# Kernel tuning notes

Measured on AMD Instinct MI355X. Metric: run time of the kernel, lower is better.

Reference implementation:

```python
import jax, jax.numpy as jnp
import numpy as np

DIM_HEAD = 32  # from init_kwargs; scale = dim_head**-0.5 per the Triton kernel


def setup_inputs() -> dict:
    key = jax.random.key(0)
    k1, k2 = jax.random.split(key)
    B, N, dim = 16, 8192, 128
    D = 4 * DIM_HEAD  # heads * dim_head
    x = jax.random.normal(k1, (B, N, dim), dtype=jnp.float32)
    # ParameterList of 16 stages, each Parameter is randn(2, dim, D) * 0.02
    qk_weights = jax.random.normal(k2, (16, 2, dim, D), dtype=jnp.float32) * 0.02
    return {"x": x, "qk_weights": qk_weights}


def reference(x, qk_weights):
    """FFT-inspired butterfly attention.

    At stage s (stride = 2**s), positions are grouped into blocks of 2*stride;
    the first `stride` elements of each block are 'a', the next `stride` are
    their butterfly partners 'b' (b = a + stride). Q/K are projected from the
    ORIGINAL x with per-stage weights; v is the running value buffer (init x).
    For each pair, a 2-way softmax over [qa.ka, qa.kb] mixes (va, vb).
    """
    B, N, dim = x.shape
    logN = int(round(np.log2(N)))
    D = qk_weights.shape[-1]
    scale = DIM_HEAD ** -0.5

    v = x
    for s in range(logN):
        stride = 1 << s
        Wq = qk_weights[s, 0]  # (dim, D)
        Wk = qk_weights[s, 1]
        q = jnp.einsum('bnd,de->bne', x, Wq) * scale  # (B,N,D)
        k = jnp.einsum('bnd,de->bne', x, Wk)
        G = N // (2 * stride)
        qr = q.reshape(B, G, 2, stride, D)
        kr = k.reshape(B, G, 2, stride, D)
        vr = v.reshape(B, G, 2, stride, dim)
        qa = qr[:, :, 0]
        ka, kb = kr[:, :, 0], kr[:, :, 1]
        va, vb = vr[:, :, 0], vr[:, :, 1]
        s_aa = jnp.sum(qa * ka, axis=-1)  # (B,G,stride)
        s_ab = jnp.sum(qa * kb, axis=-1)
        attn = jax.nn.softmax(jnp.stack([s_aa, s_ab], axis=-1), axis=-1)
        w0 = attn[..., 0:1]
        w1 = attn[..., 1:2]
        out_a = w0 * va + w1 * vb
        out_b = w1 * va + w0 * vb
        v = jnp.stack([out_a, out_b], axis=2).reshape(B, N, dim)
    return v
```

## Files before the change

### kernel.cpp

```cpp
#include <hip/hip_runtime.h>
#include <hip/hip_bf16.h>


typedef __bf16 bf16x8 __attribute__((ext_vector_type(8)));
typedef float  f32x4  __attribute__((ext_vector_type(4)));

#define XSTR 136
#define XB_BYTES  (128 * XSTR * 2)
#define PREP_LDS  (2 * XB_BYTES)
#define LDS_W     XB_BYTES

#define VSTR 132
#define LDS_MIX (128 * VSTR * 4)

#define WS_DWT_OFF (512 * 1024)
#define DWT8_BYTES (13 * 1024 * 8 * 64 * 4)
#define DWT2_BYTES (13 * 1024 * 128 * 4)
#define WS_NEED8   (WS_DWT_OFF + DWT8_BYTES)
#define WS_NEED2   (WS_DWT_OFF + DWT2_BYTES)

__device__ __forceinline__ float ubits(unsigned int u) {
    union { unsigned int u; float f; } v; v.u = u; return v.f;
}
__device__ __forceinline__ unsigned short f2bf(float f) {
    union { float f; unsigned int u; } v; v.f = f;
    unsigned int u = v.u;
    return (unsigned short)((u + 0x7fffu + ((u >> 16) & 1u)) >> 16);
}

#define DPP_MOV_F(x, ctrl) \
    __int_as_float(__builtin_amdgcn_update_dpp(0, __float_as_int(x), (ctrl), 0xF, 0xF, true))

__device__ __forceinline__ float xlane_u(float x, int u, int lane) {
    if (u == 0) return DPP_MOV_F(x, 0xB1);
    if (u == 1) return DPP_MOV_F(x, 0x4E);
    if (u == 2) return __int_as_float(__builtin_amdgcn_ds_swizzle(__float_as_int(x), 0x101F));
    if (u == 3) return __int_as_float(__builtin_amdgcn_ds_swizzle(__float_as_int(x), 0x201F));
    if (u == 4) return __int_as_float(__builtin_amdgcn_ds_swizzle(__float_as_int(x), 0x401F));
    return __int_as_float(__builtin_amdgcn_ds_bpermute((lane ^ 32) << 2, __float_as_int(x)));
}

__global__ __launch_bounds__(512)
void prep_kernel(const float* __restrict__ qkw, unsigned short* __restrict__ PT) {
    extern __shared__ char smem[];
    unsigned short* wkb = (unsigned short*)smem;
    unsigned short* wqb = (unsigned short*)(smem + XB_BYTES);
    const int s = blockIdx.x;
    const float* Wq = qkw + (size_t)s * 32768;
    const float* Wk = Wq + 16384;
    const int tid = threadIdx.x;
    const int rl = tid >> 5, c4 = tid & 31;
#pragma unroll
    for (int j = 0; j < 8; ++j) {
        int r = j * 16 + rl;
        float4 vq = ((const float4*)Wq)[r * 32 + c4];
        float4 vk = ((const float4*)Wk)[r * 32 + c4];
        ushort4 uq; uq.x = f2bf(vq.x); uq.y = f2bf(vq.y); uq.z = f2bf(vq.z); uq.w = f2bf(vq.w);
        ushort4 uk; uk.x = f2bf(vk.x); uk.y = f2bf(vk.y); uk.z = f2bf(vk.z); uk.w = f2bf(vk.w);
        *(ushort4*)(wqb + r * XSTR + c4 * 4) = uq;
        *(ushort4*)(wkb + r * XSTR + c4 * 4) = uk;
    }
    __syncthreads();
    const int lane = tid & 63, w = tid >> 6;
    const int lane15 = lane & 15, quad = lane >> 4;
    f32x4 acc[8] = {};
#pragma unroll
    for (int kk = 0; kk < 4; ++kk) {
        bf16x8 a = *(const bf16x8*)(wkb + (w * 16 + lane15) * XSTR + kk * 32 + quad * 8);
#pragma unroll
        for (int ct = 0; ct < 8; ++ct) {
            bf16x8 b = *(const bf16x8*)(wqb + (ct * 16 + lane15) * XSTR + kk * 32 + quad * 8);
            acc[ct] = __builtin_amdgcn_mfma_f32_16x16x32_bf16(a, b, acc[ct], 0, 0, 0);
        }
    }
    unsigned short* dst = PT + s * 16384;
#pragma unroll
    for (int ct = 0; ct < 8; ++ct) {
        const int kkf = ct >> 1;
        const int qf  = (ct & 1) * 2 + (lane15 >> 3);
        const int e   = lane15 & 7;
#pragma unroll
        for (int r = 0; r < 4; ++r) {
            int fi = (w * 4 + kkf) * 64 + qf * 16 + quad * 4 + r;
            dst[fi * 8 + e] = f2bf(acc[ct][r] * 0.17677669529663687f);
        }
    }
}

__device__ __forceinline__ void stage_xb(unsigned short* xb, const float* xsrc,
                                         int tid, int base, int h_off, int rstride) {
    const int rl = tid >> 5, c4 = tid & 31;
#pragma unroll
    for (int j = 0; j < 8; ++j) {
        int i  = j * 16 + rl;
        int gp = base + (i >> 6) * h_off + (i & 63) * rstride;
        float4 val = ((const float4*)xsrc)[gp * 32 + c4];
        ushort4 us; us.x = f2bf(val.x); us.y = f2bf(val.y);
        us.z = f2bf(val.z); us.w = f2bf(val.w);
        *(ushort4*)(xb + i * XSTR + c4 * 4) = us;
    }
}

template<int NS>
__global__ __launch_bounds__(512, 4)
void weights8_kernel(const float* __restrict__ xsrc,
                     const unsigned short* __restrict__ PT,
                     float* __restrict__ dwt,
                     int s0, int base_mul, int h_off, int rstride)
{
    extern __shared__ char smem[];
    unsigned short* xb = (unsigned short*)smem;

    const int tid  = threadIdx.x;
    const int b    = blockIdx.x >> 6;
    const int sub  = blockIdx.x & 63;
    const int base = b * 8192 + sub * base_mul;

    stage_xb(xb, xsrc, tid, base, h_off, rstride);

    const int lane = tid & 63, w = tid >> 6;
    const int lane15 = lane & 15, quad = lane >> 4;

    __syncthreads();

#pragma unroll
    for (int u = 0; u < NS; ++u) {
        const int t   = 1 << u;
        const int tm1 = t - 1;

        const uint4* Pf = (const uint4*)PT + (size_t)(s0 + u) * 2048;
        uint4 af[4];
#pragma unroll
        for (int kk = 0; kk < 4; ++kk)
            af[kk] = Pf[(w * 4 + kk) * 64 + lane];

        f32x4 acc[4] = {};
#pragma unroll
        for (int pg = 0; pg < 4; ++pg) {
            const int p  = pg * 16 + lane15;
            const int ar = ((p & ~tm1) << 1) | (p & tm1);
            const unsigned short* brow = xb + ar * XSTR + quad * 8;
#pragma unroll
            for (int kk = 0; kk < 4; ++kk) {
                bf16x8 bfrag = *(const bf16x8*)(brow + kk * 32);
                union { uint4 u; bf16x8 b; } av; av.u = af[kk];
                acc[pg] = __builtin_amdgcn_mfma_f32_16x16x32_bf16(av.b, bfrag, acc[pg], 0, 0, 0);
            }
        }

        float sm[4];
#pragma unroll
        for (int pg = 0; pg < 4; ++pg) {
            const int p  = pg * 16 + lane15;
            const int ar = ((p & ~tm1) << 1) | (p & tm1);
            const unsigned short* da = xb + ar * XSTR + w * 16 + quad * 4;
            const unsigned short* db = da + t * XSTR;
            uint2 ua = *(const uint2*)da;
            uint2 ub = *(const uint2*)db;
            float a0 = ubits(ua.x << 16), a1 = ubits(ua.x & 0xffff0000u);
            float a2 = ubits(ua.y << 16), a3 = ubits(ua.y & 0xffff0000u);
            float b0 = ubits(ub.x << 16), b1 = ubits(ub.x & 0xffff0000u);
            float b2 = ubits(ub.y << 16), b3 = ubits(ub.y & 0xffff0000u);
            float s = acc[pg][0] * (a0 - b0) + acc[pg][1] * (a1 - b1)
                    + acc[pg][2] * (a2 - b2) + acc[pg][3] * (a3 - b3);
            s += xlane_u(s, 4, lane);
            s += xlane_u(s, 5, lane);
            sm[pg] = s;
        }
        float v = (lane & 32) ? ((lane & 16) ? sm[3] : sm[2])
                              : ((lane & 16) ? sm[1] : sm[0]);
        dwt[(((size_t)(s0 + u) * 1024 + blockIdx.x) * 8 + w) * 64 + lane] = v;
    }
}

template<int NS>
__global__ __launch_bounds__(512, 4)
void weights2_kernel(const float* __restrict__ xsrc,
                     const unsigned short* __restrict__ PT,
                     float* __restrict__ dwt,
                     int s0, int base_mul, int h_off, int rstride)
{
    extern __shared__ char smem[];
    unsigned short* xb = (unsigned short*)smem;

    const int tid  = threadIdx.x;
    const int b    = blockIdx.x >> 6;
    const int sub  = blockIdx.x & 63;
    const int base = b * 8192 + sub * base_mul;

    stage_xb(xb, xsrc, tid, base, h_off, rstride);

    const int lane = tid & 63, w = tid >> 6;
    const int lane15 = lane & 15, quad = lane >> 4;
    const int nt = w & 3;
    const int mh = w >> 2;
    const int p  = nt * 16 + lane15;

    __syncthreads();

#pragma unroll
    for (int u = 0; u < NS; ++u) {
        const int t   = 1 << u;
        const int tm1 = t - 1;
        const int ar  = ((p & ~tm1) << 1) | (p & tm1);

        float sm = 0.f;
        {
            const uint4* Pf = (const uint4*)PT + (size_t)(s0 + u) * 2048;
            const unsigned short* brow = xb + ar * XSTR + quad * 8;
            f32x4 acc[4] = {};
#pragma unroll
            for (int kk = 0; kk < 4; ++kk) {
                bf16x8 bfrag = *(const bf16x8*)(brow + kk * 32);
#pragma unroll
                for (int mt = 0; mt < 4; ++mt) {
                    union { uint4 u; bf16x8 b; } av;
                    av.u = Pf[((mh * 4 + mt) * 4 + kk) * 64 + lane];
                    acc[mt] = __builtin_amdgcn_mfma_f32_16x16x32_bf16(av.b, bfrag, acc[mt], 0, 0, 0);
                }
            }
            const unsigned short* da = xb + ar * XSTR + mh * 64 + quad * 4;
            const unsigned short* db = da + t * XSTR;
#pragma unroll
            for (int mt = 0; mt < 4; ++mt) {
                uint2 ua = *(const uint2*)(da + mt * 16);
                uint2 ub = *(const uint2*)(db + mt * 16);
                float a0 = ubits(ua.x << 16), a1 = ubits(ua.x & 0xffff0000u);
                float a2 = ubits(ua.y << 16), a3 = ubits(ua.y & 0xffff0000u);
                float b0 = ubits(ub.x << 16), b1 = ubits(ub.x & 0xffff0000u);
                float b2 = ubits(ub.y << 16), b3 = ubits(ub.y & 0xffff0000u);
                sm += acc[mt][0] * (a0 - b0) + acc[mt][1] * (a1 - b1)
                    + acc[mt][2] * (a2 - b2) + acc[mt][3] * (a3 - b3);
            }
        }
        sm += xlane_u(sm, 4, lane);
        sm += xlane_u(sm, 5, lane);
        if (lane < 16)
            dwt[((size_t)(s0 + u) * 1024 + blockIdx.x) * 128 + mh * 64 + nt * 16 + lane] = sm;
    }
}

template<int NS, int NPART>
__global__ __launch_bounds__(512, 4)
void mix_kernel(const float* __restrict__ vsrc,
                float* __restrict__ vdst,
                const float* __restrict__ dwt,
                int s0, int base_mul, int h_off, int rstride)
{
    extern __shared__ char smem[];
    float* vbuf = (float*)smem;

    const int tid  = threadIdx.x;
    const int b    = blockIdx.x >> 6;
    const int sub  = blockIdx.x & 63;
    const int base = b * 8192 + sub * base_mul;
    const int lane = tid & 63, w = tid >> 6;
    const int rl = tid >> 5, c4 = tid & 31;

#pragma unroll
    for (int j = 0; j < 8; ++j) {
        int i  = j * 16 + rl;
        int gp = base + (i >> 6) * h_off + (i & 63) * rstride;
        float4 val = ((const float4*)vsrc)[gp * 32 + c4];
        *(float4*)(vbuf + i * VSTR + c4 * 4) = val;
    }
    __syncthreads();

    float vlo[16], vhi[16];
    {
        const float* p0 = vbuf + (2 * lane) * VSTR + w * 16;
        const float* p1 = p0 + VSTR;
#pragma unroll
        for (int j = 0; j < 4; ++j) {
            float4 a = *(const float4*)(p0 + 4 * j);
            float4 c = *(const float4*)(p1 + 4 * j);
            vlo[4*j] = a.x; vlo[4*j+1] = a.y; vlo[4*j+2] = a.z; vlo[4*j+3] = a.w;
            vhi[4*j] = c.x; vhi[4*j+1] = c.y; vhi[4*j+2] = c.z; vhi[4*j+3] = c.w;
        }
    }

#pragma unroll
    for (int u = 0; u < NS; ++u) {
        const float* dw = dwt + ((size_t)(s0 + u) * 1024 + blockIdx.x) * (NPART * 64);
        float d = 0.f;
#pragma unroll
        for (int k = 0; k < NPART; ++k) d += dw[k * 64 + lane];
        const float w0 = 1.0f / (1.0f + __expf(-d));
        if (u < NS - 1) {
            const bool isE = ((lane >> u) & 1) == 0;
            const float wk = isE ? w0 : 1.0f - w0;
#pragma unroll
            for (int j = 0; j < 16; ++j) {
                float a = vlo[j], c = vhi[j];
                float s    = a + c;
                float keep = c + wk * (a - c);
                float send = s - keep;
                float ex   = xlane_u(send, u, lane);
                vlo[j] = isE ? keep : ex;
                vhi[j] = isE ? ex : keep;
            }
        } else {
            const float w1 = 1.0f - w0;
#pragma unroll
            for (int j = 0; j < 16; ++j) {
                float a = vlo[j], c = vhi[j];
                float oa = w0 * a + w1 * c;
                vlo[j] = oa;
                vhi[j] = a + c - oa;
            }
        }
    }

    __syncthreads();

    {
        const int FU = NS - 1;
        int r0 = ((lane >> FU) << (FU + 1)) | (lane & ((1 << FU) - 1));
        int r1 = r0 + (1 << FU);
        float* q0 = vbuf + r0 * VSTR + w * 16;
        float* q1 = vbuf + r1 * VSTR + w * 16;
#pragma unroll
        for (int j = 0; j < 4; ++j) {
            float4 a; a.x = vlo[4*j]; a.y = vlo[4*j+1]; a.z = vlo[4*j+2]; a.w = vlo[4*j+3];
            float4 c; c.x = vhi[4*j]; c.y = vhi[4*j+1]; c.z = vhi[4*j+2]; c.w = vhi[4*j+3];
            *(float4*)(q0 + 4 * j) = a;
            *(float4*)(q1 + 4 * j) = c;
        }
    }
    __syncthreads();

#pragma unroll
    for (int j = 0; j < 8; ++j) {
        int i  = j * 16 + rl;
        int gp = base + (i >> 6) * h_off + (i & 63) * rstride;
        ((float4*)vdst)[gp * 32 + c4] = *(const float4*)(vbuf + i * VSTR + c4 * 4);
    }
}

extern "C" void kernel_launch(void* const* d_in, const int* in_sizes, int n_in,
                              void* d_out, int out_size, void* d_ws, size_t ws_size,
                              hipStream_t stream) {
    const float* x   = (const float*)d_in[0];
    const float* qkw = (const float*)d_in[1];
    float* out = (float*)d_out;
    unsigned short* PT = (unsigned short*)d_ws;
    float* dwt = (float*)((char*)d_ws + WS_DWT_OFF);

    (void)hipFuncSetAttribute((const void*)prep_kernel,
                              hipFuncAttributeMaxDynamicSharedMemorySize, PREP_LDS);

    prep_kernel<<<13, 512, PREP_LDS, stream>>>(qkw, PT);

    if (ws_size >= (size_t)WS_NEED8) {
        (void)hipFuncSetAttribute((const void*)weights8_kernel<7>,
                                  hipFuncAttributeMaxDynamicSharedMemorySize, LDS_W);
        (void)hipFuncSetAttribute((const void*)weights8_kernel<6>,
                                  hipFuncAttributeMaxDynamicSharedMemorySize, LDS_W);
        (void)hipFuncSetAttribute((const void*)mix_kernel<7,8>,
                                  hipFuncAttributeMaxDynamicSharedMemorySize, LDS_MIX);
        (void)hipFuncSetAttribute((const void*)mix_kernel<6,8>,
                                  hipFuncAttributeMaxDynamicSharedMemorySize, LDS_MIX);

        weights8_kernel<7><<<1024, 512, LDS_W, stream>>>(
            x, PT, dwt, 0, 128, 64, 1);
        mix_kernel<7,8><<<1024, 512, LDS_MIX, stream>>>(
            x, out, dwt, 0, 128, 64, 1);
        weights8_kernel<6><<<1024, 512, LDS_W, stream>>>(
            x, PT, dwt, 7, 2, 1, 128);
        mix_kernel<6,8><<<1024, 512, LDS_MIX, stream>>>(
            out, out, dwt, 7, 2, 1, 128);
    } else {
        (void)hipFuncSetAttribute((const void*)weights2_kernel<7>,
                                  hipFuncAttributeMaxDynamicSharedMemorySize, LDS_W);
        (void)hipFuncSetAttribute((const void*)weights2_kernel<6>,
                                  hipFuncAttributeMaxDynamicSharedMemorySize, LDS_W);
        (void)hipFuncSetAttribute((const void*)mix_kernel<7,2>,
                                  hipFuncAttributeMaxDynamicSharedMemorySize, LDS_MIX);
        (void)hipFuncSetAttribute((const void*)mix_kernel<6,2>,
                                  hipFuncAttributeMaxDynamicSharedMemorySize, LDS_MIX);

        weights2_kernel<7><<<1024, 512, LDS_W, stream>>>(
            x, PT, dwt, 0, 128, 64, 1);
        mix_kernel<7,2><<<1024, 512, LDS_MIX, stream>>>(
            x, out, dwt, 0, 128, 64, 1);
        weights2_kernel<6><<<1024, 512, LDS_W, stream>>>(
            x, PT, dwt, 7, 2, 1, 128);
        mix_kernel<6,2><<<1024, 512, LDS_MIX, stream>>>(
            out, out, dwt, 7, 2, 1, 128);
    }
}
```

Before: 223.3 us.

## Use 2x2 MFMA warp tiling, XOR-swizzled LDS, and direct global loads in mix

```diff
diff --git a/kernel.cpp b/kernel.cpp
--- a/kernel.cpp
+++ b/kernel.cpp
@@ -8,16 +8,16 @@
 #define XSTR 136
 #define XB_BYTES  (128 * XSTR * 2)
 #define PREP_LDS  (2 * XB_BYTES)
-#define LDS_W     XB_BYTES
-
-#define VSTR 132
-#define LDS_MIX (128 * VSTR * 4)
+#define LDS_W2    XB_BYTES
+
+#define XW 128
+#define LDS_W4    (128 * XW * 2)
+
+#define LDS_MIX   (128 * 128 * 4)
 
 #define WS_DWT_OFF (512 * 1024)
-#define DWT8_BYTES (13 * 1024 * 8 * 64 * 4)
-#define DWT2_BYTES (13 * 1024 * 128 * 4)
-#define WS_NEED8   (WS_DWT_OFF + DWT8_BYTES)
-#define WS_NEED2   (WS_DWT_OFF + DWT2_BYTES)
+#define DWT4_BYTES (13 * 1024 * 4 * 64 * 4)
+#define WS_NEED4   (WS_DWT_OFF + DWT4_BYTES)
 
 __device__ __forceinline__ float ubits(unsigned int u) {
     union { unsigned int u; float f; } v; v.u = u; return v.f;
@@ -27,6 +27,7 @@
     unsigned int u = v.u;
     return (unsigned short)((u + 0x7fffu + ((u >> 16) & 1u)) >> 16);
 }
+__device__ __forceinline__ int swzr(int r) { return ((r >> 1) ^ (r >> 2)) & 15; }
 
 #define DPP_MOV_F(x, ctrl) \
     __int_as_float(__builtin_amdgcn_update_dpp(0, __float_as_int(x), (ctrl), 0xF, 0xF, true))
@@ -101,9 +102,24 @@
     }
 }
 
+__device__ __forceinline__ void stage_xb_swz(unsigned short* xb, const float* xsrc,
+                                             int tid, int base, int h_off, int rstride) {
+    const int rl = tid >> 5, c4 = tid & 31;
+#pragma unroll
+    for (int j = 0; j < 8; ++j) {
+        int i  = j * 16 + rl;
+        int gp = base + (i >> 6) * h_off + (i & 63) * rstride;
+        float4 val = ((const float4*)xsrc)[gp * 32 + c4];
+        ushort4 us; us.x = f2bf(val.x); us.y = f2bf(val.y);
+        us.z = f2bf(val.z); us.w = f2bf(val.w);
+        int slot = c4 >> 1, half = c4 & 1;
+        *(ushort4*)(xb + i * XW + (((slot ^ swzr(i)) << 3) + half * 4)) = us;
+    }
+}
+
 template<int NS>
 __global__ __launch_bounds__(512, 4)
-void weights8_kernel(const float* __restrict__ xsrc,
+void weights4_kernel(const float* __restrict__ xsrc,
                      const unsigned short* __restrict__ PT,
                      float* __restrict__ dwt,
                      int s0, int base_mul, int h_off, int rstride)
@@ -116,10 +132,12 @@
     const int sub  = blockIdx.x & 63;
     const int base = b * 8192 + sub * base_mul;
 
-    stage_xb(xb, xsrc, tid, base, h_off, rstride);
+    stage_xb_swz(xb, xsrc, tid, base, h_off, rstride);
 
     const int lane = tid & 63, w = tid >> 6;
     const int lane15 = lane & 15, quad = lane >> 4;
+    const int dh = w >> 1;
+    const int ph = w & 1;
 
     __syncthreads();
 
@@ -129,47 +147,58 @@
         const int tm1 = t - 1;
 
         const uint4* Pf = (const uint4*)PT + (size_t)(s0 + u) * 2048;
-        uint4 af[4];
-#pragma unroll
-        for (int kk = 0; kk < 4; ++kk)
-            af[kk] = Pf[(w * 4 + kk) * 64 + lane];
-
-        f32x4 acc[4] = {};
-#pragma unroll
-        for (int pg = 0; pg < 4; ++pg) {
-            const int p  = pg * 16 + lane15;
+        uint4 af[2][4];
+#pragma unroll
+        for (int mt = 0; mt < 2; ++mt)
+#pragma unroll
+            for (int kk = 0; kk < 4; ++kk)
+                af[mt][kk] = Pf[((dh * 2 + mt) * 4 + kk) * 64 + lane];
+
+        f32x4 acc[2][2] = {};
+#pragma unroll
+        for (int pg = 0; pg < 2; ++pg) {
+            const int p  = (ph * 2 + pg) * 16 + lane15;
             const int ar = ((p & ~tm1) << 1) | (p & tm1);
-            const unsigned short* brow = xb + ar * XSTR + quad * 8;
+            const int swa = swzr(ar);
+            const unsigned short* brow = xb + ar * XW;
 #pragma unroll
             for (int kk = 0; kk < 4; ++kk) {
-                bf16x8 bfrag = *(const bf16x8*)(brow + kk * 32);
-                union { uint4 u; bf16x8 b; } av; av.u = af[kk];
-                acc[pg] = __builtin_amdgcn_mfma_f32_16x16x32_bf16(av.b, bfrag, acc[pg], 0, 0, 0);
-            }
-        }
-
-        float sm[4];
-#pragma unroll
-        for (int pg = 0; pg < 4; ++pg) {
-            const int p  = pg * 16 + lane15;
+                bf16x8 bfrag = *(const bf16x8*)(brow + (((kk * 4 + quad) ^ swa) << 3));
+#pragma unroll
+                for (int mt = 0; mt < 2; ++mt) {
+                    union { uint4 u; bf16x8 b; } av; av.u = af[mt][kk];
+                    acc[mt][pg] = __builtin_amdgcn_mfma_f32_16x16x32_bf16(av.b, bfrag, acc[mt][pg], 0, 0, 0);
+                }
+            }
+        }
+
+        float sm[2];
+#pragma unroll
+        for (int pg = 0; pg < 2; ++pg) {
+            const int p  = (ph * 2 + pg) * 16 + lane15;
             const int ar = ((p & ~tm1) << 1) | (p & tm1);
-            const unsigned short* da = xb + ar * XSTR + w * 16 + quad * 4;
-            const unsigned short* db = da + t * XSTR;
-            uint2 ua = *(const uint2*)da;
-            uint2 ub = *(const uint2*)db;
-            float a0 = ubits(ua.x << 16), a1 = ubits(ua.x & 0xffff0000u);
-            float a2 = ubits(ua.y << 16), a3 = ubits(ua.y & 0xffff0000u);
-            float b0 = ubits(ub.x << 16), b1 = ubits(ub.x & 0xffff0000u);
-            float b2 = ubits(ub.y << 16), b3 = ubits(ub.y & 0xffff0000u);
-            float s = acc[pg][0] * (a0 - b0) + acc[pg][1] * (a1 - b1)
-                    + acc[pg][2] * (a2 - b2) + acc[pg][3] * (a3 - b3);
+            const int br = ar + t;
+            const int swa = swzr(ar), swb = swzr(br);
+            float s = 0.f;
+#pragma unroll
+            for (int mt = 0; mt < 2; ++mt) {
+                const int slot = dh * 4 + mt * 2 + (quad >> 1);
+                uint2 ua = *(const uint2*)(xb + ar * XW + (((slot ^ swa) << 3) + (quad & 1) * 4));
+                uint2 ub = *(const uint2*)(xb + br * XW + (((slot ^ swb) << 3) + (quad & 1) * 4));
+                float a0 = ubits(ua.x << 16), a1 = ubits(ua.x & 0xffff0000u);
+                float a2 = ubits(ua.y << 16), a3 = ubits(ua.y & 0xffff0000u);
+                float b0 = ubits(ub.x << 16), b1 = ubits(ub.x & 0xffff0000u);
+                float b2 = ubits(ub.y << 16), b3 = ubits(ub.y & 0xffff0000u);
+                s += acc[mt][pg][0] * (a0 - b0) + acc[mt][pg][1] * (a1 - b1)
+                   + acc[mt][pg][2] * (a2 - b2) + acc[mt][pg][3] * (a3 - b3);
+            }
             s += xlane_u(s, 4, lane);
             s += xlane_u(s, 5, lane);
             sm[pg] = s;
         }
-        float v = (lane & 32) ? ((lane & 16) ? sm[3] : sm[2])
-                              : ((lane & 16) ? sm[1] : sm[0]);
-        dwt[(((size_t)(s0 + u) * 1024 + blockIdx.x) * 8 + w) * 64 + lane] = v;
+        float v = (lane & 16) ? sm[1] : sm[0];
+        if (lane < 32)
+            dwt[(((size_t)(s0 + u) * 1024 + blockIdx.x) * 4 + dh) * 64 + ph * 32 + (lane & 31)] = v;
     }
 }
 
@@ -257,23 +286,17 @@
     const int lane = tid & 63, w = tid >> 6;
     const int rl = tid >> 5, c4 = tid & 31;
 
-#pragma unroll
-    for (int j = 0; j < 8; ++j) {
-        int i  = j * 16 + rl;
-        int gp = base + (i >> 6) * h_off + (i & 63) * rstride;
-        float4 val = ((const float4*)vsrc)[gp * 32 + c4];
-        *(float4*)(vbuf + i * VSTR + c4 * 4) = val;
-    }
-    __syncthreads();
-
     float vlo[16], vhi[16];
     {
-        const float* p0 = vbuf + (2 * lane) * VSTR + w * 16;
-        const float* p1 = p0 + VSTR;
+        int r0 = 2 * lane, r1 = r0 + 1;
+        int gp0 = base + (r0 >> 6) * h_off + (r0 & 63) * rstride;
+        int gp1 = base + (r1 >> 6) * h_off + (r1 & 63) * rstride;
+        const float* p0 = vsrc + (size_t)gp0 * 128 + w * 16;
+        const float* p1 = vsrc + (size_t)gp1 * 128 + w * 16;
 #pragma unroll
         for (int j = 0; j < 4; ++j) {
-            float4 a = *(const float4*)(p0 + 4 * j);
-            float4 c = *(const float4*)(p1 + 4 * j);
+            float4 a = ((const float4*)p0)[j];
+            float4 c = ((const float4*)p1)[j];
             vlo[4*j] = a.x; vlo[4*j+1] = a.y; vlo[4*j+2] = a.z; vlo[4*j+3] = a.w;
             vhi[4*j] = c.x; vhi[4*j+1] = c.y; vhi[4*j+2] = c.z; vhi[4*j+3] = c.w;
         }
@@ -311,20 +334,17 @@
         }
     }
 
-    __syncthreads();
-
     {
         const int FU = NS - 1;
         int r0 = ((lane >> FU) << (FU + 1)) | (lane & ((1 << FU) - 1));
         int r1 = r0 + (1 << FU);
-        float* q0 = vbuf + r0 * VSTR + w * 16;
-        float* q1 = vbuf + r1 * VSTR + w * 16;
 #pragma unroll
         for (int j = 0; j < 4; ++j) {
             float4 a; a.x = vlo[4*j]; a.y = vlo[4*j+1]; a.z = vlo[4*j+2]; a.w = vlo[4*j+3];
             float4 c; c.x = vhi[4*j]; c.y = vhi[4*j+1]; c.z = vhi[4*j+2]; c.w = vhi[4*j+3];
-            *(float4*)(q0 + 4 * j) = a;
-            *(float4*)(q1 + 4 * j) = c;
+            int slot = w * 4 + j;
+            *(float4*)(vbuf + r0 * 128 + ((slot ^ (r0 & 31)) << 2)) = a;
+            *(float4*)(vbuf + r1 * 128 + ((slot ^ (r1 & 31)) << 2)) = c;
         }
     }
     __syncthreads();
@@ -333,7 +353,8 @@
     for (int j = 0; j < 8; ++j) {
         int i  = j * 16 + rl;
         int gp = base + (i >> 6) * h_off + (i & 63) * rstride;
-        ((float4*)vdst)[gp * 32 + c4] = *(const float4*)(vbuf + i * VSTR + c4 * 4);
+        ((float4*)vdst)[gp * 32 + c4] =
+            *(const float4*)(vbuf + i * 128 + (((c4 ^ (i & 31)) << 2)));
     }
 }
 
@@ -351,39 +372,39 @@
 
     prep_kernel<<<13, 512, PREP_LDS, stream>>>(qkw, PT);
 
-    if (ws_size >= (size_t)WS_NEED8) {
-        (void)hipFuncSetAttribute((const void*)weights8_kernel<7>,
-                                  hipFuncAttributeMaxDynamicSharedMemorySize, LDS_W);
-        (void)hipFuncSetAttribute((const void*)weights8_kernel<6>,
-                                  hipFuncAttributeMaxDynamicSharedMemorySize, LDS_W);
-        (void)hipFuncSetAttribute((const void*)mix_kernel<7,8>,
+    if (ws_size >= (size_t)WS_NEED4) {
+        (void)hipFuncSetAttribute((const void*)weights4_kernel<7>,
+                                  hipFuncAttributeMaxDynamicSharedMemorySize, LDS_W4);
+        (void)hipFuncSetAttribute((const void*)weights4_kernel<6>,
+                                  hipFuncAttributeMaxDynamicSharedMemorySize, LDS_W4);
+        (void)hipFuncSetAttribute((const void*)mix_kernel<7,4>,
                                   hipFuncAttributeMaxDynamicSharedMemorySize, LDS_MIX);
-        (void)hipFuncSetAttribute((const void*)mix_kernel<6,8>,
+        (void)hipFuncSetAttribute((const void*)mix_kernel<6,4>,
                                   hipFuncAttributeMaxDynamicSharedMemorySize, LDS_MIX);
 
-        weights8_kernel<7><<<1024, 512, LDS_W, stream>>>(
+        weights4_kernel<7><<<1024, 512, LDS_W4, stream>>>(
             x, PT, dwt, 0, 128, 64, 1);
-        mix_kernel<7,8><<<1024, 512, LDS_MIX, stream>>>(
+        mix_kernel<7,4><<<1024, 512, LDS_MIX, stream>>>(
             x, out, dwt, 0, 128, 64, 1);
-        weights8_kernel<6><<<1024, 512, LDS_W, stream>>>(
+        weights4_kernel<6><<<1024, 512, LDS_W4, stream>>>(
             x, PT, dwt, 7, 2, 1, 128);
-        mix_kernel<6,8><<<1024, 512, LDS_MIX, stream>>>(
+        mix_kernel<6,4><<<1024, 512, LDS_MIX, stream>>>(
             out, out, dwt, 7, 2, 1, 128);
     } else {
         (void)hipFuncSetAttribute((const void*)weights2_kernel<7>,
-                                  hipFuncAttributeMaxDynamicSharedMemorySize, LDS_W);
+                                  hipFuncAttributeMaxDynamicSharedMemorySize, LDS_W2);
         (void)hipFuncSetAttribute((const void*)weights2_kernel<6>,
-                                  hipFuncAttributeMaxDynamicSharedMemorySize, LDS_W);
+                                  hipFuncAttributeMaxDynamicSharedMemorySize, LDS_W2);
         (void)hipFuncSetAttribute((const void*)mix_kernel<7,2>,
                                   hipFuncAttributeMaxDynamicSharedMemorySize, LDS_MIX);
         (void)hipFuncSetAttribute((const void*)mix_kernel<6,2>,
                                   hipFuncAttributeMaxDynamicSharedMemorySize, LDS_MIX);
 
-        weights2_kernel<7><<<1024, 512, LDS_W, stream>>>(
+        weights2_kernel<7><<<1024, 512, LDS_W2, stream>>>(
             x, PT, dwt, 0, 128, 64, 1);
         mix_kernel<7,2><<<1024, 512, LDS_MIX, stream>>>(
             x, out, dwt, 0, 128, 64, 1);
-        weights2_kernel<6><<<1024, 512, LDS_W, stream>>>(
+        weights2_kernel<6><<<1024, 512, LDS_W2, stream>>>(
             x, PT, dwt, 7, 2, 1, 128);
         mix_kernel<6,2><<<1024, 512, LDS_MIX, stream>>>(
             out, out, dwt, 7, 2, 1, 128);
```

New measurement: 206.0 us. 1.08x faster.
